# Kernel tuning notes

Hardware: AMD Instinct MI355X
Metric: run time of the kernel (lower is better)

Reference implementation:

```python
import jax, jax.numpy as jnp
import numpy as np

NUM_HEADS = 32
NUM_KV_HEADS = 8
HEAD_DIM = 128
HIDDEN = 4096
BASE = 10000.0


def setup_inputs() -> dict:
    key = jax.random.key(0)
    ks = jax.random.split(key, 9)
    bs, seq = 1, 2048
    x = jax.random.normal(ks[0], (bs, seq, HIDDEN), dtype=jnp.float32)
    position_ids = jnp.broadcast_to(jnp.arange(seq, dtype=jnp.int32), (bs, seq))
    s = 1.0 / np.sqrt(HIDDEN)
    wq = jax.random.normal(ks[1], (NUM_HEADS * HEAD_DIM, HIDDEN), dtype=jnp.float32) * s
    bq = jnp.zeros((NUM_HEADS * HEAD_DIM,), dtype=jnp.float32)
    wk = jax.random.normal(ks[2], (NUM_KV_HEADS * HEAD_DIM, HIDDEN), dtype=jnp.float32) * s
    bk = jnp.zeros((NUM_KV_HEADS * HEAD_DIM,), dtype=jnp.float32)
    wv = jax.random.normal(ks[3], (NUM_KV_HEADS * HEAD_DIM, HIDDEN), dtype=jnp.float32) * s
    bv = jnp.zeros((NUM_KV_HEADS * HEAD_DIM,), dtype=jnp.float32)
    wo = jax.random.normal(ks[4], (HIDDEN, NUM_HEADS * HEAD_DIM), dtype=jnp.float32) * s
    bo = jnp.zeros((HIDDEN,), dtype=jnp.float32)
    return {"x": x, "position_ids": position_ids, "wq": wq, "bq": bq,
            "wk": wk, "bk": bk, "wv": wv, "bv": bv, "wo": wo, "bo": bo}


def _rotate_half(t):
    h = t.shape[-1] // 2
    return jnp.concatenate([-t[..., h:], t[..., :h]], axis=-1)


def _rope_cos_sin(position_ids, dtype):
    # inv_freq: (head_dim/2,)
    inv_freq = 1.0 / (BASE ** (jnp.arange(0, HEAD_DIM, 2, dtype=jnp.float32) / HEAD_DIM))
    freqs = position_ids.astype(jnp.float32)[..., None] * inv_freq  # (bs, seq, hd/2)
    emb = jnp.concatenate([freqs, freqs], axis=-1)  # (bs, seq, hd)
    return jnp.cos(emb).astype(dtype), jnp.sin(emb).astype(dtype)


def reference(x, position_ids, wq, bq, wk, bk, wv, bv, wo, bo):
    bs, seq, _ = x.shape
    g = NUM_HEADS // NUM_KV_HEADS
    # projections -> (bs, heads, seq, head_dim)
    q = (x @ wq.T + bq).reshape(bs, seq, NUM_HEADS, HEAD_DIM).transpose(0, 2, 1, 3)
    k = (x @ wk.T + bk).reshape(bs, seq, NUM_KV_HEADS, HEAD_DIM).transpose(0, 2, 1, 3)
    v = (x @ wv.T + bv).reshape(bs, seq, NUM_KV_HEADS, HEAD_DIM).transpose(0, 2, 1, 3)
    cos, sin = _rope_cos_sin(position_ids, x.dtype)
    cos, sin = cos[:, None], sin[:, None]  # broadcast over heads
    q = q * cos + _rotate_half(q) * sin
    k = k * cos + _rotate_half(k) * sin
    # grouped attention without expanding kv (same math as repeat_kv)
    qg = q.reshape(bs, NUM_KV_HEADS, g, seq, HEAD_DIM)
    scores = jnp.einsum('bhgqd,bhkd->bhgqk', qg, k) / jnp.sqrt(
        jnp.asarray(HEAD_DIM, dtype=jnp.float32)).astype(x.dtype)
    probs = jax.nn.softmax(scores.astype(jnp.float32), axis=-1).astype(x.dtype)
    out = jnp.einsum('bhgqk,bhkd->bhgqd', probs, v)  # (bs, kvh, g, seq, hd)
    out = out.reshape(bs, NUM_HEADS, seq, HEAD_DIM).transpose(0, 2, 1, 3)
    out = out.reshape(bs, seq, NUM_HEADS * HEAD_DIM)
    return out @ wo.T + bo
```

## Files before the change

kernel.cpp:

```cpp
#include <hip/hip_runtime.h>
#include <stdint.h>

typedef unsigned short u16;
typedef unsigned long long u64;
typedef __attribute__((ext_vector_type(8))) short s8v;
typedef __attribute__((ext_vector_type(4))) float f4v;

#define MFMA(a, b, c) __builtin_amdgcn_mfma_f32_16x16x32_bf16((a), (b), (c), 0, 0, 0)

__device__ __forceinline__ u16 f2b(float f) {
  uint32_t x = __float_as_uint(f);
  x += 0x7fff + ((x >> 16) & 1);
  return (u16)(x >> 16);
}
__device__ __forceinline__ float b2f(u16 u) {
  return __uint_as_float(((uint32_t)u) << 16);
}

__device__ __forceinline__ void gll16(const void* g, void* l) {
  __builtin_amdgcn_global_load_lds((const __attribute__((address_space(1))) uint32_t*)g,
                                   (__attribute__((address_space(3))) uint32_t*)l, 16, 0, 0);
}
__device__ __forceinline__ void bar() { __builtin_amdgcn_s_barrier(); }

__global__ void cvt_all(const float* __restrict__ x, const float* __restrict__ wq,
                        const float* __restrict__ wk, const float* __restrict__ wv,
                        const float* __restrict__ wo,
                        u16* __restrict__ xb, u16* __restrict__ wqkv, u16* __restrict__ wob) {
  int i = blockIdx.x * 256 + threadIdx.x;
  const float* s; u16* d; size_t off;
  if      (i < 1048576) { s = x;  d = xb;   off = (size_t)i; }
  else if (i < 3145728) { s = wq; d = wqkv; off = (size_t)(i - 1048576); }
  else if (i < 3670016) { s = wk; d = wqkv + (size_t)16777216; off = (size_t)(i - 3145728); }
  else if (i < 4194304) { s = wv; d = wqkv + (size_t)20971520; off = (size_t)(i - 3670016); }
  else                  { s = wo; d = wob;  off = (size_t)(i - 4194304); }
  const float4* sp = (const float4*)(s + off * 8);
  float4 f0 = sp[0], f1 = sp[1];
  s8v o;
  o[0] = (short)f2b(f0.x); o[1] = (short)f2b(f0.y); o[2] = (short)f2b(f0.z); o[3] = (short)f2b(f0.w);
  o[4] = (short)f2b(f1.x); o[5] = (short)f2b(f1.y); o[6] = (short)f2b(f1.z); o[7] = (short)f2b(f1.w);
  *(s8v*)(d + off * 8) = o;
}

template <int BM, int MODE>
__global__ __launch_bounds__(512, 2) void gemm8p(
    const u16* __restrict__ A, const u16* __restrict__ Bact,
    const float* __restrict__ bias,
    float* __restrict__ Cf, u16* __restrict__ Cq, u16* __restrict__ Ck, u16* __restrict__ Cv,
    int K) {
  extern __shared__ u16 smem[];
  constexpr int AO = BM * 64;
  constexpr int BE = 2 * BM * 64;
  constexpr int BO = BE + 16384;
  constexpr int MI = BM / 64;
  constexpr int NH = BM / 64;

  const int tid = threadIdx.x;
  const int l = tid & 63, wv = tid >> 6;
  const int wm = wv >> 2, wn = wv & 3;
  const int lr = l & 15, lg = l >> 4;
  const int swz = 16 * (lr & 7);
  const int wrow = wm * (BM / 2);

  const int nwg = gridDim.x;
  int bid = blockIdx.x;
  bid = (bid & 7) * (nwg >> 3) + (bid >> 3);
  const int NB = 8;
  const int m0 = (bid / NB) * BM, n0 = (bid % NB) * 256;

  const size_t K64 = (size_t)64 * K;

  const int sr = tid >> 3;
  const int sc = ((tid & 7) ^ (sr & 7)) * 8;
  const u16* gA = A + (size_t)(m0 + sr) * K + sc;
  const u16* gB = Bact + (size_t)(n0 + sr) * K + sc;

  auto STA = [&](int P, int h, int kt) {
    gll16(gA + (size_t)(h * 64) * K + (size_t)kt * 64,
          smem + (P ? AO : 0) + h * 4096 + tid * 8);
  };
  auto STB = [&](int P, int h, int kt) {
    const u16* g = gB + (size_t)(h * 128) * K + (size_t)kt * 64;
    u16* d = smem + (P ? BO : BE) + h * 8192 + tid * 8;
    gll16(g, d);
    gll16(g + K64, d + 4096);
  };

  const char* smc = (const char*)smem;
  s8v a[MI][2], b0[2][2], b1[2][2];
  auto LDA = [&](int P, int QR) {
#pragma unroll
    for (int mi = 0; mi < MI; ++mi)
#pragma unroll
      for (int kk = 0; kk < 2; ++kk)
        a[mi][kk] = *(const s8v*)(smc + (P ? AO * 2 : 0) +
            (wrow + QR * (BM / 4) + mi * 16 + lr) * 128 + ((kk * 64 + lg * 16) ^ swz));
  };
  auto LDB = [&](int P, int QC, s8v bb[2][2]) {
#pragma unroll
    for (int ni = 0; ni < 2; ++ni)
#pragma unroll
      for (int kk = 0; kk < 2; ++kk)
        bb[ni][kk] = *(const s8v*)(smc + (P ? BO * 2 : BE * 2) +
            (wn * 64 + QC * 32 + ni * 16 + lr) * 128 + ((kk * 64 + lg * 16) ^ swz));
  };

  f4v acc[BM / 32][4];
#pragma unroll
  for (int i = 0; i < BM / 32; ++i)
#pragma unroll
    for (int j = 0; j < 4; ++j) acc[i][j] = {0.f, 0.f, 0.f, 0.f};

#define PHMF(QR, QC, B)                                                        \
  _Pragma("unroll") for (int mi = 0; mi < MI; ++mi)                            \
    _Pragma("unroll") for (int ni = 0; ni < 2; ++ni)                           \
      _Pragma("unroll") for (int kk = 0; kk < 2; ++kk)                         \
        acc[(QR) * MI + mi][(QC) * 2 + ni] =                                   \
            MFMA(a[mi][kk], B[ni][kk], acc[(QR) * MI + mi][(QC) * 2 + ni]);

  STB(0, 0, 0); STB(0, 1, 0);
#pragma unroll
  for (int h = 0; h < NH; ++h) STA(0, h, 0);
  STB(1, 0, 1); STB(1, 1, 1);
  asm volatile("s_waitcnt vmcnt(4)" ::: "memory");
  bar();

  const int ITERS = K >> 7;
  for (int i = 0; i < ITERS; ++i) {
    const int kn = 2 * i + 2;
    const bool more = (i + 1 < ITERS);
    LDA(0, 0); LDB(0, 0, b0); LDB(0, 1, b1);
    STA(1, 0, 2 * i + 1); STA(1, 1, 2 * i + 1);
    bar();
    __builtin_amdgcn_s_setprio(1);
    PHMF(0, 0, b0); PHMF(0, 1, b1);
    __builtin_amdgcn_s_setprio(0);
    bar();
    LDA(0, 1);
    if constexpr (NH > 2) STA(1, 2, 2 * i + 1);
    if (more) { STB(0, 0, kn); STB(0, 1, kn); }
    bar();
    __builtin_amdgcn_s_setprio(1);
    PHMF(1, 1, b1); PHMF(1, 0, b0);
    __builtin_amdgcn_s_setprio(0);
    if (more) asm volatile("s_waitcnt vmcnt(4)" ::: "memory");
    else      asm volatile("s_waitcnt vmcnt(0)" ::: "memory");
    bar();
    LDA(1, 0); LDB(1, 0, b0); LDB(1, 1, b1);
    if (more) { STA(0, 0, kn); STA(0, 1, kn); }
    bar();
    __builtin_amdgcn_s_setprio(1);
    PHMF(0, 0, b0); PHMF(0, 1, b1);
    __builtin_amdgcn_s_setprio(0);
    bar();
    LDA(1, 1);
    if (more) {
      if constexpr (NH > 2) STA(0, 2, kn);
      STB(1, 0, 2 * i + 3); STB(1, 1, 2 * i + 3);
    }
    bar();
    __builtin_amdgcn_s_setprio(1);
    PHMF(1, 1, b1); PHMF(1, 0, b0);
    __builtin_amdgcn_s_setprio(0);
    asm volatile("s_waitcnt vmcnt(4)" ::: "memory");
    bar();
  }
#undef PHMF

  bar();

  if constexpr (MODE == 2) {
#pragma unroll
    for (int fi = 0; fi < BM / 32; ++fi) {
      const int f0 = m0 + wrow + fi * 16;
      if (f0 >= 5120) {
#pragma unroll
        for (int fj = 0; fj < 4; ++fj)
#pragma unroll
          for (int r = 0; r < 4; ++r) {
            const int f = f0 + lg * 4 + r;
            const int tok = n0 + wn * 64 + fj * 16 + lr;
            Cv[(size_t)(f - 5120) * 2048 + tok] = f2b(acc[fi][fj][r] + bias[f]);
          }
      }
    }
    if (m0 + wrow < 5120) {
      u16* buf = smem + wv * 3328;
#pragma unroll
      for (int c = 0; c < 2; ++c) {
#pragma unroll
        for (int fj2 = 0; fj2 < 2; ++fj2) {
          const int fj = 2 * c + fj2;
          const int tl = fj2 * 16 + lr;
#pragma unroll
          for (int fi = 0; fi < BM / 32; ++fi) {
            const int f0 = m0 + wrow + fi * 16;
            if (f0 < 5120) {
#pragma unroll
              for (int r = 0; r < 4; ++r) {
                const int fl = fi * 16 + lg * 4 + r;
                buf[tl * 104 + fl] = f2b(acc[fi][fj][r] + bias[m0 + wrow + fl]);
              }
            }
          }
        }
        asm volatile("s_waitcnt lgkmcnt(0)" ::: "memory");
        const int row = l >> 1, half = l & 1;
        const int tok = n0 + wn * 64 + c * 32 + row;
#pragma unroll
        for (int i2 = 0; i2 < 6; ++i2) {
          const int flc = (2 * i2 + half) * 8;
          const int f = m0 + wrow + flc;
          if (f < 4096)
            *(s8v*)(Cq + (size_t)tok * 4096 + f) = *(const s8v*)(buf + row * 104 + flc);
          else if (f < 5120)
            *(s8v*)(Ck + (size_t)tok * 1024 + (f - 4096)) = *(const s8v*)(buf + row * 104 + flc);
        }
        asm volatile("s_waitcnt lgkmcnt(0)" ::: "memory");
        bar();
      }
    } else {
      bar(); bar();
    }
  } else {
    float* buf = (float*)smem + wv * 1088;
#pragma unroll
    for (int c = 0; c < 4; ++c) {
#pragma unroll
      for (int fi = 0; fi < BM / 32; ++fi)
#pragma unroll
        for (int r = 0; r < 4; ++r) {
          const int fl = fi * 16 + lg * 4 + r;
          buf[lr * 68 + fl] = acc[fi][c][r] + bias[m0 + wrow + fl];
        }
      asm volatile("s_waitcnt lgkmcnt(0)" ::: "memory");
      const int row = l >> 2, q4 = l & 3;
      const int tok = n0 + wn * 64 + c * 16 + row;
      float* g = Cf + (size_t)tok * 4096 + m0 + wrow + q4 * 16;
      const float* src = buf + row * 68 + q4 * 16;
#pragma unroll
      for (int i2 = 0; i2 < 4; ++i2)
        *(f4v*)(g + i2 * 4) = *(const f4v*)(src + i2 * 4);
      asm volatile("s_waitcnt lgkmcnt(0)" ::: "memory");
    }
  }
}

__global__ void rope_kernel(u16* __restrict__ q, u16* __restrict__ k, const int* __restrict__ pos) {
  int i = blockIdx.x * 256 + threadIdx.x;
  const int NQ = 2048 * 32 * 64;
  const int NK = 2048 * 8 * 64;
  u16* buf;
  int m, d, stride, h;
  if (i < NQ) { buf = q; m = i >> 11; h = (i >> 6) & 31; d = i & 63; stride = 4096; }
  else {
    i -= NQ; if (i >= NK) return;
    buf = k; m = i >> 9; h = (i >> 6) & 7; d = i & 63; stride = 1024;
  }
  size_t base = (size_t)m * stride + h * 128 + d;
  float a = b2f(buf[base]), b = b2f(buf[base + 64]);
  float p = (float)pos[m];
  float ang = p * exp2f(-0.20762050593045952f * (float)d);
  float s, c;
  sincosf(ang, &s, &c);
  buf[base]      = f2b(a * c - b * s);
  buf[base + 64] = f2b(b * c + a * s);
}

__global__ __launch_bounds__(256, 2) void attn_kernel(const u16* __restrict__ Q, const u16* __restrict__ Kb,
                                                      const u16* __restrict__ Vt, u16* __restrict__ Ao) {
  __shared__ __align__(16) u16 Ks[64 * 128];
  __shared__ __align__(16) u16 Vs[128 * 64];
  __shared__ __align__(16) u16 Ps[4][32 * 64];
  const int tid = threadIdx.x;
  const int l = tid & 63, wv = tid >> 6;
  const int lr = l & 15, lg = l >> 4;
  const int head = blockIdx.x >> 4, qt = blockIdx.x & 15;
  const int kh = head >> 2;
  const int qrow = qt * 128 + wv * 32 + lr;

  s8v qf[2][4];
#pragma unroll
  for (int qh = 0; qh < 2; ++qh)
#pragma unroll
    for (int s = 0; s < 4; ++s)
      qf[qh][s] = *(const s8v*)&Q[(size_t)(qrow + qh * 16) * 4096 + head * 128 + s * 32 + lg * 8];

  f4v zero = {0.f, 0.f, 0.f, 0.f};
  f4v ao[2][8];
#pragma unroll
  for (int qh = 0; qh < 2; ++qh)
#pragma unroll
    for (int tt = 0; tt < 8; ++tt) ao[qh][tt] = zero;
  float mrun[2] = {-1e30f, -1e30f}, lrun[2] = {0.f, 0.f};

  const u16* Kg = Kb + kh * 128;
  const u16* Vg = Vt + (size_t)(kh * 128) * 2048;
  const u16* kp[4];
  const u16* vp[4];
#pragma unroll
  for (int p = 0; p < 4; ++p) {
    const int ki = tid + 256 * p;
    const int kr = ki >> 4, kc = (ki & 15) ^ (kr & 7);
    kp[p] = Kg + (size_t)kr * 1024 + kc * 8;
    const int vr = ki >> 3, vc = (ki & 7) ^ (vr & 7);
    vp[p] = Vg + (size_t)vr * 2048 + vc * 8;
  }

  char* KsB = (char*)Ks;
  char* VsB = (char*)Vs;
  char* PwB = (char*)Ps[wv];
  const int swz = 16 * (lr & 7);
  const float C2 = 0.12753102f;

  for (int t = 0; t < 2048; t += 64) {
    __syncthreads();
#pragma unroll
    for (int p = 0; p < 4; ++p) {
      gll16(kp[p] + (size_t)t * 1024, KsB + (tid + 256 * p) * 16);
      gll16(vp[p] + t,                VsB + (tid + 256 * p) * 16);
    }
    __syncthreads();

    f4v c[2][4];
#pragma unroll
    for (int qh = 0; qh < 2; ++qh)
#pragma unroll
      for (int j = 0; j < 4; ++j) c[qh][j] = zero;
#pragma unroll
    for (int s = 0; s < 4; ++s) {
#pragma unroll
      for (int j = 0; j < 4; ++j) {
        s8v kf = *(const s8v*)(KsB + (16 * j + lr) * 256 + (((4 * s + lg) * 16) ^ swz));
        c[0][j] = MFMA(kf, qf[0][s], c[0][j]);
        c[1][j] = MFMA(kf, qf[1][s], c[1][j]);
      }
    }

#pragma unroll
    for (int qh = 0; qh < 2; ++qh) {
      float mx = fmaxf(fmaxf(c[qh][0][0], c[qh][0][1]), fmaxf(c[qh][0][2], c[qh][0][3]));
#pragma unroll
      for (int j = 1; j < 4; ++j)
        mx = fmaxf(mx, fmaxf(fmaxf(c[qh][j][0], c[qh][j][1]), fmaxf(c[qh][j][2], c[qh][j][3])));
      mx = fmaxf(mx, __shfl_xor(mx, 16));
      mx = fmaxf(mx, __shfl_xor(mx, 32));
      float m2x = mx * C2;

      if (!__all(m2x - mrun[qh] <= 8.f)) {
        float mnew = fmaxf(mrun[qh], m2x);
        float alpha = __builtin_amdgcn_exp2f(mrun[qh] - mnew);
        float ar[4];
#pragma unroll
        for (int r = 0; r < 4; ++r) ar[r] = __shfl(alpha, 4 * lg + r);
#pragma unroll
        for (int tt = 0; tt < 8; ++tt)
#pragma unroll
          for (int r = 0; r < 4; ++r) ao[qh][tt][r] *= ar[r];
        lrun[qh] *= alpha;
        mrun[qh] = mnew;
      }

      float rs = 0.f;
#pragma unroll
      for (int j = 0; j < 4; ++j) {
        float p0 = __builtin_amdgcn_exp2f(__builtin_fmaf(c[qh][j][0], C2, -mrun[qh]));
        float p1 = __builtin_amdgcn_exp2f(__builtin_fmaf(c[qh][j][1], C2, -mrun[qh]));
        float p2 = __builtin_amdgcn_exp2f(__builtin_fmaf(c[qh][j][2], C2, -mrun[qh]));
        float p3 = __builtin_amdgcn_exp2f(__builtin_fmaf(c[qh][j][3], C2, -mrun[qh]));
        rs += (p0 + p1) + (p2 + p3);
        uint32_t lo = (uint32_t)f2b(p0) | ((uint32_t)f2b(p1) << 16);
        uint32_t hi = (uint32_t)f2b(p2) | ((uint32_t)f2b(p3) << 16);
        u64 pak = (u64)lo | ((u64)hi << 32);
        *(u64*)(PwB + (qh * 16 + lr) * 128 + ((32 * j + 8 * lg) ^ swz)) = pak;
      }
      rs += __shfl_xor(rs, 16);
      rs += __shfl_xor(rs, 32);
      lrun[qh] += rs;
    }

#pragma unroll
    for (int h = 0; h < 2; ++h) {
      s8v pf0 = *(const s8v*)(PwB + lr * 128 + ((64 * h + 16 * lg) ^ swz));
      s8v pf1 = *(const s8v*)(PwB + (16 + lr) * 128 + ((64 * h + 16 * lg) ^ swz));
#pragma unroll
      for (int tt = 0; tt < 8; ++tt) {
        s8v vf = *(const s8v*)(VsB + (16 * tt + lr) * 128 + (((4 * h + lg) * 16) ^ swz));
        ao[0][tt] = MFMA(pf0, vf, ao[0][tt]);
        ao[1][tt] = MFMA(pf1, vf, ao[1][tt]);
      }
    }
  }

#pragma unroll
  for (int qh = 0; qh < 2; ++qh) {
    float inv = 1.f / lrun[qh];
    float ir[4];
#pragma unroll
    for (int r = 0; r < 4; ++r) ir[r] = __shfl(inv, 4 * lg + r);
#pragma unroll
    for (int tt = 0; tt < 8; ++tt)
#pragma unroll
      for (int r = 0; r < 4; ++r)
        Ao[(size_t)(qt * 128 + wv * 32 + qh * 16 + 4 * lg + r) * 4096 + head * 128 + 16 * tt + lr] =
            f2b(ao[qh][tt][r] * ir[r]);
  }
}

extern "C" void kernel_launch(void* const* d_in, const int* in_sizes, int n_in,
                              void* d_out, int out_size, void* d_ws, size_t ws_size,
                              hipStream_t stream) {
  const float* x  = (const float*)d_in[0];
  const int*   pos = (const int*)d_in[1];
  const float* wq = (const float*)d_in[2];
  const float* bq = (const float*)d_in[3];
  const float* wk = (const float*)d_in[4];
  const float* bk = (const float*)d_in[5];
  const float* wv = (const float*)d_in[6];
  const float* bv = (const float*)d_in[7];
  const float* wo = (const float*)d_in[8];
  const float* bo = (const float*)d_in[9];
  float* out = (float*)d_out;

  char* ws = (char*)d_ws;
  u16* xb   = (u16*)(ws + 0);
  u16* wqkv = (u16*)(ws + 16777216);
  u16* wob  = (u16*)(ws + 67108864);
  u16* qb   = (u16*)(ws + 100663296);
  u16* kb   = (u16*)(ws + 117440512);
  u16* vT   = (u16*)(ws + 121634816);
  u16* ab   = (u16*)(ws + 125829120);
  float* bqkv = (float*)(ws + 142606336);

  hipMemcpyAsync(bqkv,        bq, 4096 * sizeof(float), hipMemcpyDeviceToDevice, stream);
  hipMemcpyAsync(bqkv + 4096, bk, 1024 * sizeof(float), hipMemcpyDeviceToDevice, stream);
  hipMemcpyAsync(bqkv + 5120, bv, 1024 * sizeof(float), hipMemcpyDeviceToDevice, stream);

  cvt_all<<<24576, 256, 0, stream>>>(x, wq, wk, wv, wo, xb, wqkv, wob);

  gemm8p<192, 2><<<256, 512, 114688, stream>>>(wqkv, xb, bqkv,
                                               nullptr, qb, kb, vT, 4096);
  rope_kernel<<<(2048 * 32 * 64 + 2048 * 8 * 64) / 256, 256, 0, stream>>>(qb, kb, pos);
  attn_kernel<<<512, 256, 0, stream>>>(qb, kb, vT, ab);
  gemm8p<128, 0><<<256, 512, 98304, stream>>>(wob, ab, bo,
                                              out, nullptr, nullptr, nullptr, 4096);
}
```

Measured before the change: 325.6 us.

## Replace 8-wave GEMM with 4-wave kernel using smaller M tiles

Both GEMMs now use a new 256-thread kernel with half-height M tiles (96 for QKV, 64 for the output projection) and twice as many blocks. A is double-buffered, while B is a single buffer refilled after its fragments are read. Each 64-wide K step ends with a full vmcnt(0) wait instead of the deeper 8-phase software pipeline. The aim is smaller blocks, better occupancy and simpler scheduling. The cost is less load/compute overlap and less data reuse per block.

```diff
diff --git a/kernel.cpp b/kernel.cpp
--- a/kernel.cpp
+++ b/kernel.cpp
@@ -43,7 +43,7 @@
 }
 
 template <int BM, int MODE>
-__global__ __launch_bounds__(512, 2) void gemm8p(
+__global__ __launch_bounds__(256, 2) void gemm2p(
     const u16* __restrict__ A, const u16* __restrict__ Bact,
     const float* __restrict__ bias,
     float* __restrict__ Cf, u16* __restrict__ Cq, u16* __restrict__ Ck, u16* __restrict__ Cv,
@@ -51,16 +51,13 @@
   extern __shared__ u16 smem[];
   constexpr int AO = BM * 64;
   constexpr int BE = 2 * BM * 64;
-  constexpr int BO = BE + 16384;
-  constexpr int MI = BM / 64;
-  constexpr int NH = BM / 64;
+  constexpr int MI = BM / 32;
+  constexpr int AR = BM / 16;
 
   const int tid = threadIdx.x;
   const int l = tid & 63, wv = tid >> 6;
-  const int wm = wv >> 2, wn = wv & 3;
   const int lr = l & 15, lg = l >> 4;
   const int swz = 16 * (lr & 7);
-  const int wrow = wm * (BM / 2);
 
   const int nwg = gridDim.x;
   int bid = blockIdx.x;
@@ -68,22 +65,20 @@
   const int NB = 8;
   const int m0 = (bid / NB) * BM, n0 = (bid % NB) * 256;
 
-  const size_t K64 = (size_t)64 * K;
-
   const int sr = tid >> 3;
   const int sc = ((tid & 7) ^ (sr & 7)) * 8;
   const u16* gA = A + (size_t)(m0 + sr) * K + sc;
   const u16* gB = Bact + (size_t)(n0 + sr) * K + sc;
 
   auto STA = [&](int P, int h, int kt) {
-    gll16(gA + (size_t)(h * 64) * K + (size_t)kt * 64,
-          smem + (P ? AO : 0) + h * 4096 + tid * 8);
+    gll16(gA + (size_t)(h * 32) * K + (size_t)kt * 64,
+          smem + (P ? AO : 0) + h * 2048 + tid * 8);
   };
-  auto STB = [&](int P, int h, int kt) {
-    const u16* g = gB + (size_t)(h * 128) * K + (size_t)kt * 64;
-    u16* d = smem + (P ? BO : BE) + h * 8192 + tid * 8;
-    gll16(g, d);
-    gll16(g + K64, d + 4096);
+  auto STB = [&](int kt) {
+#pragma unroll
+    for (int rr = 0; rr < 8; ++rr)
+      gll16(gB + (size_t)(rr * 32) * K + (size_t)kt * 64,
+            smem + BE + rr * 2048 + tid * 8);
   };
 
   const char* smc = (const char*)smem;
@@ -94,76 +89,56 @@
 #pragma unroll
       for (int kk = 0; kk < 2; ++kk)
         a[mi][kk] = *(const s8v*)(smc + (P ? AO * 2 : 0) +
-            (wrow + QR * (BM / 4) + mi * 16 + lr) * 128 + ((kk * 64 + lg * 16) ^ swz));
+            (QR * (BM / 2) + mi * 16 + lr) * 128 + ((kk * 64 + lg * 16) ^ swz));
   };
-  auto LDB = [&](int P, int QC, s8v bb[2][2]) {
+  auto LDB = [&](int QC, s8v bb[2][2]) {
 #pragma unroll
     for (int ni = 0; ni < 2; ++ni)
 #pragma unroll
       for (int kk = 0; kk < 2; ++kk)
-        bb[ni][kk] = *(const s8v*)(smc + (P ? BO * 2 : BE * 2) +
-            (wn * 64 + QC * 32 + ni * 16 + lr) * 128 + ((kk * 64 + lg * 16) ^ swz));
+        bb[ni][kk] = *(const s8v*)(smc + BE * 2 +
+            (wv * 64 + QC * 32 + ni * 16 + lr) * 128 + ((kk * 64 + lg * 16) ^ swz));
   };
 
-  f4v acc[BM / 32][4];
-#pragma unroll
-  for (int i = 0; i < BM / 32; ++i)
+  f4v acc[AR][4];
+#pragma unroll
+  for (int i = 0; i < AR; ++i)
 #pragma unroll
     for (int j = 0; j < 4; ++j) acc[i][j] = {0.f, 0.f, 0.f, 0.f};
 
 #define PHMF(QR, QC, B)                                                        \
+  __builtin_amdgcn_s_setprio(1);                                               \
   _Pragma("unroll") for (int mi = 0; mi < MI; ++mi)                            \
     _Pragma("unroll") for (int ni = 0; ni < 2; ++ni)                           \
       _Pragma("unroll") for (int kk = 0; kk < 2; ++kk)                         \
         acc[(QR) * MI + mi][(QC) * 2 + ni] =                                   \
-            MFMA(a[mi][kk], B[ni][kk], acc[(QR) * MI + mi][(QC) * 2 + ni]);
-
-  STB(0, 0, 0); STB(0, 1, 0);
-#pragma unroll
-  for (int h = 0; h < NH; ++h) STA(0, h, 0);
-  STB(1, 0, 1); STB(1, 1, 1);
-  asm volatile("s_waitcnt vmcnt(4)" ::: "memory");
+            MFMA(a[mi][kk], B[ni][kk], acc[(QR) * MI + mi][(QC) * 2 + ni]);    \
+  __builtin_amdgcn_s_setprio(0);
+
+#pragma unroll
+  for (int h = 0; h < MI; ++h) STA(0, h, 0);
+  STB(0);
+  asm volatile("s_waitcnt vmcnt(0)" ::: "memory");
   bar();
 
-  const int ITERS = K >> 7;
+  const int ITERS = K >> 6;
   for (int i = 0; i < ITERS; ++i) {
-    const int kn = 2 * i + 2;
+    const int P = i & 1;
     const bool more = (i + 1 < ITERS);
-    LDA(0, 0); LDB(0, 0, b0); LDB(0, 1, b1);
-    STA(1, 0, 2 * i + 1); STA(1, 1, 2 * i + 1);
+    LDA(P, 0); LDB(0, b0); LDB(1, b1);
+    if (more) {
+#pragma unroll
+      for (int h = 0; h < MI; ++h) STA(P ^ 1, h, i + 1);
+    }
     bar();
-    __builtin_amdgcn_s_setprio(1);
     PHMF(0, 0, b0); PHMF(0, 1, b1);
-    __builtin_amdgcn_s_setprio(0);
     bar();
-    LDA(0, 1);
-    if constexpr (NH > 2) STA(1, 2, 2 * i + 1);
-    if (more) { STB(0, 0, kn); STB(0, 1, kn); }
+    LDA(P, 1);
+    if (more) STB(i + 1);
     bar();
-    __builtin_amdgcn_s_setprio(1);
     PHMF(1, 1, b1); PHMF(1, 0, b0);
-    __builtin_amdgcn_s_setprio(0);
-    if (more) asm volatile("s_waitcnt vmcnt(4)" ::: "memory");
-    else      asm volatile("s_waitcnt vmcnt(0)" ::: "memory");
+    asm volatile("s_waitcnt vmcnt(0)" ::: "memory");
     bar();
-    LDA(1, 0); LDB(1, 0, b0); LDB(1, 1, b1);
-    if (more) { STA(0, 0, kn); STA(0, 1, kn); }
-    bar();
-    __builtin_amdgcn_s_setprio(1);
-    PHMF(0, 0, b0); PHMF(0, 1, b1);
-    __builtin_amdgcn_s_setprio(0);
-    bar();
-    LDA(1, 1);
-    if (more) {
-      if constexpr (NH > 2) STA(0, 2, kn);
-      STB(1, 0, 2 * i + 3); STB(1, 1, 2 * i + 3);
-    }
-    bar();
-    __builtin_amdgcn_s_setprio(1);
-    PHMF(1, 1, b1); PHMF(1, 0, b0);
-    __builtin_amdgcn_s_setprio(0);
-    asm volatile("s_waitcnt vmcnt(4)" ::: "memory");
-    bar();
   }
 #undef PHMF
 
@@ -171,20 +146,20 @@
 
   if constexpr (MODE == 2) {
 #pragma unroll
-    for (int fi = 0; fi < BM / 32; ++fi) {
-      const int f0 = m0 + wrow + fi * 16;
+    for (int ai = 0; ai < AR; ++ai) {
+      const int f0 = m0 + ai * 16;
       if (f0 >= 5120) {
 #pragma unroll
         for (int fj = 0; fj < 4; ++fj)
 #pragma unroll
           for (int r = 0; r < 4; ++r) {
             const int f = f0 + lg * 4 + r;
-            const int tok = n0 + wn * 64 + fj * 16 + lr;
-            Cv[(size_t)(f - 5120) * 2048 + tok] = f2b(acc[fi][fj][r] + bias[f]);
+            const int tok = n0 + wv * 64 + fj * 16 + lr;
+            Cv[(size_t)(f - 5120) * 2048 + tok] = f2b(acc[ai][fj][r] + bias[f]);
           }
       }
     }
-    if (m0 + wrow < 5120) {
+    if (m0 < 5120) {
       u16* buf = smem + wv * 3328;
 #pragma unroll
       for (int c = 0; c < 2; ++c) {
@@ -193,50 +168,47 @@
           const int fj = 2 * c + fj2;
           const int tl = fj2 * 16 + lr;
 #pragma unroll
-          for (int fi = 0; fi < BM / 32; ++fi) {
-            const int f0 = m0 + wrow + fi * 16;
+          for (int ai = 0; ai < AR; ++ai) {
+            const int f0 = m0 + ai * 16;
             if (f0 < 5120) {
 #pragma unroll
               for (int r = 0; r < 4; ++r) {
-                const int fl = fi * 16 + lg * 4 + r;
-                buf[tl * 104 + fl] = f2b(acc[fi][fj][r] + bias[m0 + wrow + fl]);
+                const int fl = ai * 16 + lg * 4 + r;
+                buf[tl * 104 + fl] = f2b(acc[ai][fj][r] + bias[m0 + fl]);
               }
             }
           }
         }
         asm volatile("s_waitcnt lgkmcnt(0)" ::: "memory");
         const int row = l >> 1, half = l & 1;
-        const int tok = n0 + wn * 64 + c * 32 + row;
-#pragma unroll
-        for (int i2 = 0; i2 < 6; ++i2) {
+        const int tok = n0 + wv * 64 + c * 32 + row;
+#pragma unroll
+        for (int i2 = 0; i2 < AR; ++i2) {
           const int flc = (2 * i2 + half) * 8;
-          const int f = m0 + wrow + flc;
+          const int f = m0 + flc;
           if (f < 4096)
             *(s8v*)(Cq + (size_t)tok * 4096 + f) = *(const s8v*)(buf + row * 104 + flc);
           else if (f < 5120)
             *(s8v*)(Ck + (size_t)tok * 1024 + (f - 4096)) = *(const s8v*)(buf + row * 104 + flc);
         }
         asm volatile("s_waitcnt lgkmcnt(0)" ::: "memory");
-        bar();
-      }
-    } else {
-      bar(); bar();
+      }
     }
   } else {
     float* buf = (float*)smem + wv * 1088;
 #pragma unroll
     for (int c = 0; c < 4; ++c) {
 #pragma unroll
-      for (int fi = 0; fi < BM / 32; ++fi)
+      for (int ai = 0; ai < AR; ++ai)
 #pragma unroll
         for (int r = 0; r < 4; ++r) {
-          const int fl = fi * 16 + lg * 4 + r;
-          buf[lr * 68 + fl] = acc[fi][c][r] + bias[m0 + wrow + fl];
+          const int fl = ai * 16 + lg * 4 + r;
+          buf[lr * 68 + fl] = acc[ai][c][r] + bias[m0 + fl];
         }
       asm volatile("s_waitcnt lgkmcnt(0)" ::: "memory");
       const int row = l >> 2, q4 = l & 3;
-      const int tok = n0 + wn * 64 + c * 16 + row;
-      float* g = Cf + (size_t)tok * 4096 + m0 + wrow + q4 * 16;
+      const int tok = n0 + wv * 64 + c * 16 + row;
+      float* g = Cf + (size_t)tok * 4096 + m0 + q4 * 16;
       const float* src = buf + row * 68 + q4 * 16;
 #pragma unroll
       for (int i2 = 0; i2 < 4; ++i2)
@@ -438,10 +410,10 @@
 
   cvt_all<<<24576, 256, 0, stream>>>(x, wq, wk, wv, wo, xb, wqkv, wob);
 
-  gemm8p<192, 2><<<256, 512, 114688, stream>>>(wqkv, xb, bqkv,
-                                               nullptr, qb, kb, vT, 4096);
+  gemm2p<96, 2><<<512, 256, 57344, stream>>>(wqkv, xb, bqkv,
+                                             nullptr, qb, kb, vT, 4096);
   rope_kernel<<<(2048 * 32 * 64 + 2048 * 8 * 64) / 256, 256, 0, stream>>>(qb, kb, pos);
   attn_kernel<<<512, 256, 0, stream>>>(qb, kb, vT, ab);
-  gemm8p<128, 0><<<256, 512, 98304, stream>>>(wob, ab, bo,
-                                              out, nullptr, nullptr, nullptr, 4096);
-}
+  gemm2p<64, 0><<<512, 256, 49152, stream>>>(wob, ab, bo,
+                                             out, nullptr, nullptr, nullptr, 4096);
+}
```

New measurement: 328.5 us. Within noise of the previous version (+0.9%).

## Replace output projection GEMM with smaller-tile two-blocks-per-CU kernel

Applied to the files above, without the earlier changes.

Adds a new 256-thread GEMM kernel (gemm2p) with 64x256 tiles, a double-buffered A tile and launch bounds allowing two blocks per CU, and uses it for the output projection instead of the 512-thread 128-row kernel. This doubles the grid to 512 blocks to improve occupancy and latency hiding on the final GEMM. In exchange, B tiles are single-buffered and the loop has more barriers per iteration, and reuse per block is lower. The old template is explicitly instantiated so it stays compiled.

```diff
diff --git a/kernel.cpp b/kernel.cpp
--- a/kernel.cpp
+++ b/kernel.cpp
@@ -246,6 +246,9 @@
   }
 }
 
+template __global__ void gemm8p<128, 0>(const u16*, const u16*, const float*,
+                                        float*, u16*, u16*, u16*, int);
+
 __global__ void rope_kernel(u16* __restrict__ q, u16* __restrict__ k, const int* __restrict__ pos) {
   int i = blockIdx.x * 256 + threadIdx.x;
   const int NQ = 2048 * 32 * 64;
@@ -407,6 +410,133 @@
   }
 }
 
+template <int BM, int MODE>
+__global__ __launch_bounds__(256, 2) void gemm2p(
+    const u16* __restrict__ A, const u16* __restrict__ Bact,
+    const float* __restrict__ bias,
+    float* __restrict__ Cf, u16* __restrict__ Cq, u16* __restrict__ Ck, u16* __restrict__ Cv,
+    int K) {
+  extern __shared__ u16 smem[];
+  constexpr int AO = BM * 64;
+  constexpr int BE = 2 * BM * 64;
+  constexpr int MI = BM / 32;
+  constexpr int AR = BM / 16;
+
+  const int tid = threadIdx.x;
+  const int l = tid & 63, wv = tid >> 6;
+  const int lr = l & 15, lg = l >> 4;
+  const int swz = 16 * (lr & 7);
+
+  const int nwg = gridDim.x;
+  int bid = blockIdx.x;
+  bid = (bid & 7) * (nwg >> 3) + (bid >> 3);
+  const int NB = 8;
+  const int m0 = (bid / NB) * BM, n0 = (bid % NB) * 256;
+
+  const int sr = tid >> 3;
+  const int sc = ((tid & 7) ^ (sr & 7)) * 8;
+  const u16* gA = A + (size_t)(m0 + sr) * K + sc;
+  const u16* gB = Bact + (size_t)(n0 + sr) * K + sc;
+
+  auto STA = [&](int P, int h, int kt) {
+    gll16(gA + (size_t)(h * 32) * K + (size_t)kt * 64,
+          smem + (P ? AO : 0) + h * 2048 + tid * 8);
+  };
+  auto STB = [&](int kt) {
+#pragma unroll
+    for (int rr = 0; rr < 8; ++rr)
+      gll16(gB + (size_t)(rr * 32) * K + (size_t)kt * 64,
+            smem + BE + rr * 2048 + tid * 8);
+  };
+
+  const char* smc = (const char*)smem;
+  s8v a[MI][2], b0[2][2], b1[2][2];
+  auto LDA = [&](int P, int QR) {
+#pragma unroll
+    for (int mi = 0; mi < MI; ++mi)
+#pragma unroll
+      for (int kk = 0; kk < 2; ++kk)
+        a[mi][kk] = *(const s8v*)(smc + (P ? AO * 2 : 0) +
+            (QR * (BM / 2) + mi * 16 + lr) * 128 + ((kk * 64 + lg * 16) ^ swz));
+  };
+  auto LDB = [&](int QC, s8v bb[2][2]) {
+#pragma unroll
+    for (int ni = 0; ni < 2; ++ni)
+#pragma unroll
+      for (int kk = 0; kk < 2; ++kk)
+        bb[ni][kk] = *(const s8v*)(smc + BE * 2 +
+            (wv * 64 + QC * 32 + ni * 16 + lr) * 128 + ((kk * 64 + lg * 16) ^ swz));
+  };
+
+  f4v acc[AR][4];
+#pragma unroll
+  for (int i = 0; i < AR; ++i)
+#pragma unroll
+    for (int j = 0; j < 4; ++j) acc[i][j] = {0.f, 0.f, 0.f, 0.f};
+
+#define PHMF(QR, QC, B)                                                        \
+  __builtin_amdgcn_s_setprio(1);                                               \
+  _Pragma("unroll") for (int mi = 0; mi < MI; ++mi)                            \
+    _Pragma("unroll") for (int ni = 0; ni < 2; ++ni)                           \
+      _Pragma("unroll") for (int kk = 0; kk < 2; ++kk)                         \
+        acc[(QR) * MI + mi][(QC) * 2 + ni] =                                   \
+            MFMA(a[mi][kk], B[ni][kk], acc[(QR) * MI + mi][(QC) * 2 + ni]);    \
+  __builtin_amdgcn_s_setprio(0);
+
+#pragma unroll
+  for (int h = 0; h < MI; ++h) STA(0, h, 0);
+  STB(0);
+  asm volatile("s_waitcnt vmcnt(0)" ::: "memory");
+  bar();
+
+  const int ITERS = K >> 6;
+  for (int i = 0; i < ITERS; ++i) {
+    const int P = i & 1;
+    const bool more = (i + 1 < ITERS);
+    LDA(P, 0); LDB(0, b0); LDB(1, b1);
+    if (more) {
+#pragma unroll
+      for (int h = 0; h < MI; ++h) STA(P ^ 1, h, i + 1);
+    }
+    bar();
+    PHMF(0, 0, b0); PHMF(0, 1, b1);
+    bar();
+    LDA(P, 1);
+    if (more) STB(i + 1);
+    bar();
+    PHMF(1, 1, b1); PHMF(1, 0, b0);
+    asm volatile("s_waitcnt vmcnt(0)" ::: "memory");
+    bar();
+  }
+#undef PHMF
+
+  bar();
+
+  if constexpr (MODE == 2) {
+  } else {
+    float* buf = (float*)smem + wv * 1088;
+#pragma unroll
+    for (int c = 0; c < 4; ++c) {
+#pragma unroll
+      for (int ai = 0; ai < AR; ++ai)
+#pragma unroll
+        for (int r = 0; r < 4; ++r) {
+          const int fl = ai * 16 + lg * 4 + r;
+          buf[lr * 68 + fl] = acc[ai][c][r] + bias[m0 + fl];
+        }
+      asm volatile("s_waitcnt lgkmcnt(0)" ::: "memory");
+      const int row = l >> 2, q4 = l & 3;
+      const int tok = n0 + wv * 64 + c * 16 + row;
+      float* g = Cf + (size_t)tok * 4096 + m0 + q4 * 16;
+      const float* src = buf + row * 68 + q4 * 16;
+#pragma unroll
+      for (int i2 = 0; i2 < 4; ++i2)
+        *(f4v*)(g + i2 * 4) = *(const f4v*)(src + i2 * 4);
+      asm volatile("s_waitcnt lgkmcnt(0)" ::: "memory");
+    }
+  }
+}
+
 extern "C" void kernel_launch(void* const* d_in, const int* in_sizes, int n_in,
                               void* d_out, int out_size, void* d_ws, size_t ws_size,
                               hipStream_t stream) {
@@ -442,6 +572,6 @@
                                                nullptr, qb, kb, vT, 4096);
   rope_kernel<<<(2048 * 32 * 64 + 2048 * 8 * 64) / 256, 256, 0, stream>>>(qb, kb, pos);
   attn_kernel<<<512, 256, 0, stream>>>(qb, kb, vT, ab);
-  gemm8p<128, 0><<<256, 512, 98304, stream>>>(wob, ab, bo,
-                                              out, nullptr, nullptr, nullptr, 4096);
-}
+  gemm2p<64, 0><<<512, 256, 49152, stream>>>(wob, ab, bo,
+                                             out, nullptr, nullptr, nullptr, 4096);
+}
```

Result: no change. 328.9 us (+1.0%).
